# Kernel tuning notes

Hardware: AMD Instinct MI355X
Metric: run time of the kernel (lower is better)

## Reference

```python
import jax, jax.numpy as jnp
import numpy as np

B, N, T, FM = 2, 768, 96, 8
HID = 64
TD = HID // 2   # temporal_dim = max(8, 32) = 32
MD = HID // 2   # mark_hidden_dim = 32


def _lin_init(key, fan_in, fan_out):
    k1, k2 = jax.random.split(key)
    bound = 1.0 / np.sqrt(fan_in)
    w = jax.random.uniform(k1, (fan_in, fan_out), minval=-bound, maxval=bound, dtype=jnp.float32)
    b = jax.random.uniform(k2, (fan_out,), minval=-bound, maxval=bound, dtype=jnp.float32)
    return w, b


def setup_inputs() -> dict:
    key = jax.random.key(0)
    ks = jax.random.split(key, 16)
    x_hist = jax.random.normal(ks[0], (B, N, T), dtype=jnp.float32)
    x_mark = jax.random.normal(ks[1], (B, N, T, FM), dtype=jnp.float32)
    a_static = jax.random.uniform(ks[2], (N, N), dtype=jnp.float32)
    te_w1, te_b1 = _lin_init(ks[3], 3, TD)
    te_w2, te_b2 = _lin_init(ks[4], TD, TD)
    me_w1, me_b1 = _lin_init(ks[5], FM, MD)
    me_w2, me_b2 = _lin_init(ks[6], MD, MD)
    nf_w, nf_b = _lin_init(ks[7], TD + MD, HID)
    ps_w1, ps_b1 = _lin_init(ks[8], 3 * HID, HID)
    ps_w2, ps_b2 = _lin_init(ks[9], HID, 1)
    raw_lambda = jnp.array([np.log(0.1 / 0.9)], dtype=jnp.float32)  # logit(lambda_init)
    return dict(x_hist=x_hist, x_mark=x_mark, a_static=a_static,
                te_w1=te_w1, te_b1=te_b1, te_w2=te_w2, te_b2=te_b2,
                me_w1=me_w1, me_b1=me_b1, me_w2=me_w2, me_b2=me_b2,
                nf_w=nf_w, nf_b=nf_b,
                ps_w1=ps_w1, ps_b1=ps_b1, ps_w2=ps_w2, ps_b2=ps_b2,
                raw_lambda=raw_lambda)


def reference(x_hist, x_mark, a_static,
              te_w1, te_b1, te_w2, te_b2,
              me_w1, me_b1, me_w2, me_b2,
              nf_w, nf_b, ps_w1, ps_b1, ps_w2, ps_b2, raw_lambda):
    n = x_hist.shape[1]
    # temporal stats: last / mean / max over T -> [B,N,3]
    stats = jnp.stack([x_hist[:, :, -1], x_hist.mean(axis=-1), x_hist.max(axis=-1)], axis=-1)
    h_t = jax.nn.relu(stats @ te_w1 + te_b1) @ te_w2 + te_b2          # [B,N,TD]
    mark_sum = x_mark.mean(axis=2)                                    # [B,N,FM]
    h_m = jax.nn.relu(mark_sum @ me_w1 + me_b1) @ me_w2 + me_b2       # [B,N,MD]
    h = jax.nn.relu(jnp.concatenate([h_t, h_m], axis=-1) @ nf_w + nf_b)  # [B,N,H]
    # pair scorer: Linear([h_i, h_j, |h_i-h_j|]) decomposed over the 3 blocks
    hdim = h.shape[-1]
    w_i, w_j, w_d = ps_w1[:hdim], ps_w1[hdim:2 * hdim], ps_w1[2 * hdim:]
    s_i = h @ w_i                                                     # [B,N,H]
    s_j = h @ w_j                                                     # [B,N,H]
    diff = jnp.abs(h[:, :, None, :] - h[:, None, :, :])               # [B,N,N,H]
    pre = s_i[:, :, None, :] + s_j[:, None, :, :] + diff @ w_d + ps_b1
    delta = jnp.tanh((jax.nn.relu(pre) @ ps_w2 + ps_b2)[..., 0])      # [B,N,N]
    eye = jnp.eye(n, dtype=delta.dtype)
    delta = delta * (1.0 - eye)
    delta = 0.5 * (delta + jnp.swapaxes(delta, 1, 2))                 # sym_graph
    lam = jax.nn.sigmoid(raw_lambda)                                  # [1]
    a_hybrid = a_static[None] + lam * delta
    a_hybrid = jax.nn.relu(a_hybrid)                                  # nonneg_mode='relu'
    d = jnp.clip(a_hybrid.sum(axis=-1, keepdims=True), 1e-6, None)    # row norm
    a_hybrid = a_hybrid / d
    return a_hybrid, lam
```

## Files before the change

kernel.cpp:

```cpp
#include <hip/hip_runtime.h>
#include <hip/hip_bf16.h>
#include <math.h>

#define B_ 2
#define N_ 768
#define T_ 96
#define FM_ 8
#define HID_ 64
#define TD_ 32
#define MD_ 32
#define TILE 16
#define NTILES (N_/TILE)
#define NTP (NTILES*(NTILES+1)/2)
#define SSTR 68

typedef __attribute__((ext_vector_type(8))) short short8v;
typedef __attribute__((ext_vector_type(4))) float f32x4;
typedef __attribute__((ext_vector_type(4))) unsigned int uint4v;

__device__ __forceinline__ unsigned int pack_bf2(float d0, float d1){
  __hip_bfloat162 t = __float22bfloat162_rn(make_float2(d0, d1));
  unsigned int u;
  __builtin_memcpy(&u, &t, 4);
  return u;
}

__device__ __forceinline__ float ftanh(float x){
  float e = __expf(2.f * x);
  return 1.f - 2.f * __builtin_amdgcn_rcpf(e + 1.f);
}

__device__ __forceinline__ float wave_sum64(float v){
  #pragma unroll
  for (int m = 32; m; m >>= 1) v += __shfl_xor(v, m);
  return v;
}
__device__ __forceinline__ float wave_max64(float v){
  #pragma unroll
  for (int m = 32; m; m >>= 1) v = fmaxf(v, __shfl_xor(v, m));
  return v;
}

__global__ __launch_bounds__(64) void feat_kernel(
    const float* __restrict__ x_hist, const float* __restrict__ x_mark,
    const float* __restrict__ te_w1, const float* __restrict__ te_b1,
    const float* __restrict__ te_w2, const float* __restrict__ te_b2,
    const float* __restrict__ me_w1, const float* __restrict__ me_b1,
    const float* __restrict__ me_w2, const float* __restrict__ me_b2,
    const float* __restrict__ nf_w,  const float* __restrict__ nf_b,
    const float* __restrict__ ps_w1,
    float* __restrict__ h_out, float* __restrict__ si_out, float* __restrict__ sj_out,
    unsigned short* __restrict__ wdf)
{
  const int lane = threadIdx.x;

  if (blockIdx.x >= B_ * N_) {
    const int q  = blockIdx.x - B_ * N_;
    const int nt = q >> 1, s = q & 1;
    const int col = (lane & 15) + 16 * nt;
    const int k0  = s * 32 + ((lane >> 4) << 3);
    #pragma unroll
    for (int jj = 0; jj < 8; ++jj) {
      float v = ps_w1[(2 * HID_ + k0 + jj) * HID_ + col];
      __hip_bfloat16 bv = __float2bfloat16(v);
      unsigned short us;
      __builtin_memcpy(&us, &bv, 2);
      wdf[(q * 64 + lane) * 8 + jj] = us;
    }
    return;
  }

  const int row = blockIdx.x;

  __shared__ float st[3];
  __shared__ float ms[FM_];
  __shared__ float t1s[TD_];
  __shared__ float m1s[MD_];
  __shared__ float hc[HID_];
  __shared__ float hs[HID_];

  const float* xh = x_hist + (long)row * T_;
  float s  = xh[lane];
  float mx = s;
  if (lane < T_ - 64) { float v = xh[lane + 64]; s += v; mx = fmaxf(mx, v); }
  s  = wave_sum64(s);
  mx = wave_max64(mx);
  if (lane == 0) { st[0] = xh[T_ - 1]; st[1] = s * (1.0f / T_); st[2] = mx; }

  const float* xm = x_mark + (long)row * T_ * FM_;
  float msv = 0.f;
  #pragma unroll
  for (int k = 0; k < 12; ++k) msv += xm[lane + 64 * k];
  msv += __shfl_xor(msv, 8);
  msv += __shfl_xor(msv, 16);
  msv += __shfl_xor(msv, 32);
  if (lane < FM_) ms[lane] = msv * (1.0f / T_);
  __syncthreads();

  if (lane < TD_) {
    float a = te_b1[lane];
    #pragma unroll
    for (int k = 0; k < 3; ++k) a += st[k] * te_w1[k * TD_ + lane];
    t1s[lane] = fmaxf(a, 0.f);
    float am = me_b1[lane];
    #pragma unroll
    for (int k = 0; k < FM_; ++k) am += ms[k] * me_w1[k * MD_ + lane];
    m1s[lane] = fmaxf(am, 0.f);
  }
  __syncthreads();
  if (lane < TD_) {
    float a = te_b2[lane];
    #pragma unroll
    for (int k = 0; k < TD_; ++k) a += t1s[k] * te_w2[k * TD_ + lane];
    hc[lane] = a;
    float am = me_b2[lane];
    #pragma unroll
    for (int k = 0; k < MD_; ++k) am += m1s[k] * me_w2[k * MD_ + lane];
    hc[TD_ + lane] = am;
  }
  __syncthreads();
  {
    float a = nf_b[lane];
    #pragma unroll
    for (int k = 0; k < HID_; ++k) a += hc[k] * nf_w[k * HID_ + lane];
    float hv = fmaxf(a, 0.f);
    hs[lane] = hv;
    h_out[(long)row * HID_ + lane] = hv;
  }
  __syncthreads();
  {
    float a1 = 0.f, a2 = 0.f;
    #pragma unroll
    for (int k = 0; k < HID_; ++k) {
      float hv = hs[k];
      a1 += hv * ps_w1[k * HID_ + lane];
      a2 += hv * ps_w1[(HID_ + k) * HID_ + lane];
    }
    si_out[(long)row * HID_ + lane] = a1;
    sj_out[(long)row * HID_ + lane] = a2;
  }
}

__global__ __launch_bounds__(256) void pair_kernel(
    const float* __restrict__ h, const float* __restrict__ si, const float* __restrict__ sj,
    const float* __restrict__ ps_b1, const float* __restrict__ ps_w2,
    const float* __restrict__ ps_b2, const unsigned short* __restrict__ wdf,
    float* __restrict__ delta)
{
  int bidx = blockIdx.x;
  int b  = bidx / NTP;
  int tp = bidx % NTP;
  int tI = 0;
  while (tp >= NTILES - tI) { tp -= NTILES - tI; ++tI; }
  int tJ = tI + tp;
  const int i0 = tI * TILE, j0 = tJ * TILE;

  __shared__ float hI  [TILE][HID_];
  __shared__ float hJT [HID_][TILE + 1];
  __shared__ float SIIb[TILE][SSTR];
  __shared__ float SJI_[TILE][SSTR];
  __shared__ float SIJb[TILE][SSTR];
  __shared__ float SJJ_[TILE][SSTR];
  __shared__ float w2s [HID_];

  const int tid  = threadIdx.x;
  const int lane = tid & 63;
  const int w    = tid >> 6;

  {
    const int r  = tid >> 4;
    const int c4 = (tid & 15) * 4;
    const f32x4 b14 = *(const f32x4*)(ps_b1 + c4);
    const long gi = ((long)b * N_ + i0 + r) * HID_ + c4;
    const long gj = ((long)b * N_ + j0 + r) * HID_ + c4;
    f32x4 vhi = *(const f32x4*)(h  + gi);
    f32x4 vhj = *(const f32x4*)(h  + gj);
    f32x4 vii = *(const f32x4*)(si + gi);
    f32x4 vji = *(const f32x4*)(sj + gi);
    f32x4 vij = *(const f32x4*)(si + gj);
    f32x4 vjj = *(const f32x4*)(sj + gj);
    *(f32x4*)&hI  [r][c4] = vhi;
    #pragma unroll
    for (int q = 0; q < 4; ++q) hJT[c4 + q][r] = vhj[q];
    *(f32x4*)&SIIb[r][c4] = vii + b14;
    *(f32x4*)&SJI_[r][c4] = vji;
    *(f32x4*)&SIJb[r][c4] = vij + b14;
    *(f32x4*)&SJJ_[r][c4] = vjj;
    if (tid < 16) *(f32x4*)&w2s[tid * 4] = *(const f32x4*)(ps_w2 + tid * 4);
  }
  const float b2 = ps_b2[0];
  __syncthreads();

  const int g   = lane >> 4;
  const int c16 = lane & 15;

  short8v wfr[8];
  const short8v* wdp = (const short8v*)wdf;
  #pragma unroll
  for (int q = 0; q < 8; ++q) wfr[q] = wdp[q * 64 + lane];

  float hJv[2][8];
  #pragma unroll
  for (int s = 0; s < 2; ++s)
    #pragma unroll
    for (int jj = 0; jj < 8; ++jj)
      hJv[s][jj] = hJT[32 * s + 8 * g + jj][c16];

  float* drow = delta + (long)b * N_ * N_;

  #pragma unroll
  for (int m = 0; m < 4; ++m) {
    const int iloc = w * 4 + m;
    const int i = i0 + iloc;

    short8v afr[2];
    #pragma unroll
    for (int s = 0; s < 2; ++s) {
      f32x4 ha = *(const f32x4*)&hI[iloc][32 * s + 8 * g];
      f32x4 hb = *(const f32x4*)&hI[iloc][32 * s + 8 * g + 4];
      uint4v uv;
      #pragma unroll
      for (int p = 0; p < 2; ++p) {
        float d0 = fabsf(ha[2*p]   - hJv[s][2*p]);
        float d1 = fabsf(ha[2*p+1] - hJv[s][2*p+1]);
        uv[p] = pack_bf2(d0, d1);
      }
      #pragma unroll
      for (int p = 0; p < 2; ++p) {
        float d0 = fabsf(hb[2*p]   - hJv[s][4 + 2*p]);
        float d1 = fabsf(hb[2*p+1] - hJv[s][4 + 2*p+1]);
        uv[2 + p] = pack_bf2(d0, d1);
      }
      afr[s] = __builtin_bit_cast(short8v, uv);
    }

    f32x4 acc[4];
    #pragma unroll
    for (int mt = 0; mt < 4; ++mt) acc[mt] = (f32x4){0.f, 0.f, 0.f, 0.f};
    #pragma unroll
    for (int s = 0; s < 2; ++s)
      #pragma unroll
      for (int mt = 0; mt < 4; ++mt)
        acc[mt] = __builtin_amdgcn_mfma_f32_16x16x32_bf16(wfr[2 * mt + s], afr[s], acc[mt], 0, 0, 0);

    float a1 = 0.f, a2 = 0.f;
    #pragma unroll
    for (int mt = 0; mt < 4; ++mt) {
      const int cb = 16 * mt + 4 * g;
      f32x4 sII4 = *(const f32x4*)&SIIb[iloc][cb];
      f32x4 sJI4 = *(const f32x4*)&SJI_[iloc][cb];
      f32x4 sJJ4 = *(const f32x4*)&SJJ_[c16][cb];
      f32x4 sIJ4 = *(const f32x4*)&SIJb[c16][cb];
      f32x4 w24  = *(const f32x4*)&w2s[cb];
      #pragma unroll
      for (int r = 0; r < 4; ++r) {
        float av = acc[mt][r];
        a1 += fmaxf(av + sII4[r] + sJJ4[r], 0.f) * w24[r];
        a2 += fmaxf(av + sJI4[r] + sIJ4[r], 0.f) * w24[r];
      }
    }
    a1 += __shfl_xor(a1, 16);  a1 += __shfl_xor(a1, 32);
    a2 += __shfl_xor(a2, 16);  a2 += __shfl_xor(a2, 32);

    if (g == 0) {
      const int j = j0 + c16;
      float sym = 0.5f * (ftanh(a1 + b2) + ftanh(a2 + b2));
      float val = (i == j) ? 0.f : sym;
      drow[(long)i * N_ + j] = val;
      drow[(long)j * N_ + i] = val;
    }
  }
}

__global__ __launch_bounds__(256) void norm_kernel(
    const float* __restrict__ a_static, const float* __restrict__ raw_lambda,
    float* __restrict__ out)
{
  const int row = blockIdx.x;
  const int i   = row % N_;
  const int tid = threadIdx.x;
  const float lam = 1.f / (1.f + expf(-raw_lambda[0]));

  const float* arow = a_static + (long)i * N_;
  float* drow = out + (long)row * N_;

  float vals[3];
  float s = 0.f;
  #pragma unroll
  for (int r = 0; r < 3; ++r) {
    int j = r * 256 + tid;
    float v = arow[j] + lam * drow[j];
    v = fmaxf(v, 0.f);
    vals[r] = v;
    s += v;
  }
  s = wave_sum64(s);
  __shared__ float ps[4];
  if ((tid & 63) == 0) ps[tid >> 6] = s;
  __syncthreads();
  float tot = ps[0] + ps[1] + ps[2] + ps[3];
  float inv = 1.f / fmaxf(tot, 1e-6f);
  #pragma unroll
  for (int r = 0; r < 3; ++r) {
    int j = r * 256 + tid;
    drow[j] = vals[r] * inv;
  }
  if (row == 0 && tid == 0) out[(long)B_ * N_ * N_] = lam;
}

extern "C" void kernel_launch(void* const* d_in, const int* in_sizes, int n_in,
                              void* d_out, int out_size, void* d_ws, size_t ws_size,
                              hipStream_t stream) {
  const float* x_hist     = (const float*)d_in[0];
  const float* x_mark     = (const float*)d_in[1];
  const float* a_static   = (const float*)d_in[2];
  const float* te_w1      = (const float*)d_in[3];
  const float* te_b1      = (const float*)d_in[4];
  const float* te_w2      = (const float*)d_in[5];
  const float* te_b2      = (const float*)d_in[6];
  const float* me_w1      = (const float*)d_in[7];
  const float* me_b1      = (const float*)d_in[8];
  const float* me_w2      = (const float*)d_in[9];
  const float* me_b2      = (const float*)d_in[10];
  const float* nf_w       = (const float*)d_in[11];
  const float* nf_b       = (const float*)d_in[12];
  const float* ps_w1      = (const float*)d_in[13];
  const float* ps_b1      = (const float*)d_in[14];
  const float* ps_w2      = (const float*)d_in[15];
  const float* ps_b2      = (const float*)d_in[16];
  const float* raw_lambda = (const float*)d_in[17];

  float* out = (float*)d_out;
  float* h   = (float*)d_ws;
  float* si  = h  + (long)B_ * N_ * HID_;
  float* sj  = si + (long)B_ * N_ * HID_;
  unsigned short* wdf = (unsigned short*)(sj + (long)B_ * N_ * HID_);

  feat_kernel<<<B_ * N_ + 8, 64, 0, stream>>>(
      x_hist, x_mark, te_w1, te_b1, te_w2, te_b2,
      me_w1, me_b1, me_w2, me_b2, nf_w, nf_b, ps_w1, h, si, sj, wdf);

  pair_kernel<<<B_ * NTP, 256, 0, stream>>>(
      h, si, sj, ps_b1, ps_w2, ps_b2, wdf, out);

  norm_kernel<<<B_ * N_, 256, 0, stream>>>(a_static, raw_lambda, out);
}
```

Before: 35.97 us.

## Use 32x16 pair tiles with hoisted per-column operands in pair kernel

The pair kernel now covers a 32-row by 16-column tile per block, so each wave handles 8 rows instead of 4. The grid is re-enumerated over upper-triangular 32x16 tiles, giving 600 blocks per batch instead of 1176. The column-side scorer terms and w2 fragments are loaded into registers once, outside the row loop, and a launch-bounds occupancy hint is added. Writes are restricted to i<j plus the diagonal, which removes duplicate stores from tiles that straddle the diagonal. The costs are more registers, more shared memory per block, and fewer blocks available to spread across the GPU.

Measured after the change: 35.60 us. Within noise of the previous version (-1.0%).

```diff
diff --git a/kernel.cpp b/kernel.cpp
--- a/kernel.cpp
+++ b/kernel.cpp
@@ -10,8 +10,9 @@
 #define TD_ 32
 #define MD_ 32
 #define TILE 16
+#define TI32 32
 #define NTILES (N_/TILE)
-#define NTP (NTILES*(NTILES+1)/2)
+#define PERB 600
 #define SSTR 68
 
 typedef __attribute__((ext_vector_type(8))) short short8v;
@@ -141,24 +142,24 @@
   }
 }
 
-__global__ __launch_bounds__(256) void pair_kernel(
+__global__ __launch_bounds__(256, 3) void pair_kernel(
     const float* __restrict__ h, const float* __restrict__ si, const float* __restrict__ sj,
     const float* __restrict__ ps_b1, const float* __restrict__ ps_w2,
     const float* __restrict__ ps_b2, const unsigned short* __restrict__ wdf,
     float* __restrict__ delta)
 {
   int bidx = blockIdx.x;
-  int b  = bidx / NTP;
-  int tp = bidx % NTP;
-  int tI = 0;
-  while (tp >= NTILES - tI) { tp -= NTILES - tI; ++tI; }
-  int tJ = tI + tp;
-  const int i0 = tI * TILE, j0 = tJ * TILE;
-
-  __shared__ float hI  [TILE][HID_];
+  int b = bidx / PERB;
+  int t = bidx % PERB;
+  int a = 0;
+  while (t >= NTILES - 2 * a) { t -= NTILES - 2 * a; ++a; }
+  int tJ = 2 * a + t;
+  const int i0 = a * TI32, j0 = tJ * TILE;
+
+  __shared__ float hI  [TI32][HID_];
   __shared__ float hJT [HID_][TILE + 1];
-  __shared__ float SIIb[TILE][SSTR];
-  __shared__ float SJI_[TILE][SSTR];
+  __shared__ float SIIb[TI32][SSTR];
+  __shared__ float SJI_[TI32][SSTR];
   __shared__ float SIJb[TILE][SSTR];
   __shared__ float SJJ_[TILE][SSTR];
   __shared__ float w2s [HID_];
@@ -171,21 +172,20 @@
     const int r  = tid >> 4;
     const int c4 = (tid & 15) * 4;
     const f32x4 b14 = *(const f32x4*)(ps_b1 + c4);
-    const long gi = ((long)b * N_ + i0 + r) * HID_ + c4;
+    #pragma unroll
+    for (int p = 0; p < 2; ++p) {
+      const int rr = r + p * 16;
+      const long gi = ((long)b * N_ + i0 + rr) * HID_ + c4;
+      *(f32x4*)&hI  [rr][c4] = *(const f32x4*)(h  + gi);
+      *(f32x4*)&SIIb[rr][c4] = *(const f32x4*)(si + gi) + b14;
+      *(f32x4*)&SJI_[rr][c4] = *(const f32x4*)(sj + gi);
+    }
     const long gj = ((long)b * N_ + j0 + r) * HID_ + c4;
-    f32x4 vhi = *(const f32x4*)(h  + gi);
-    f32x4 vhj = *(const f32x4*)(h  + gj);
-    f32x4 vii = *(const f32x4*)(si + gi);
-    f32x4 vji = *(const f32x4*)(sj + gi);
-    f32x4 vij = *(const f32x4*)(si + gj);
-    f32x4 vjj = *(const f32x4*)(sj + gj);
-    *(f32x4*)&hI  [r][c4] = vhi;
+    f32x4 vhj = *(const f32x4*)(h + gj);
     #pragma unroll
     for (int q = 0; q < 4; ++q) hJT[c4 + q][r] = vhj[q];
-    *(f32x4*)&SIIb[r][c4] = vii + b14;
-    *(f32x4*)&SJI_[r][c4] = vji;
-    *(f32x4*)&SIJb[r][c4] = vij + b14;
-    *(f32x4*)&SJJ_[r][c4] = vjj;
+    *(f32x4*)&SIJb[r][c4] = *(const f32x4*)(si + gj) + b14;
+    *(f32x4*)&SJJ_[r][c4] = *(const f32x4*)(sj + gj);
     if (tid < 16) *(f32x4*)&w2s[tid * 4] = *(const f32x4*)(ps_w2 + tid * 4);
   }
   const float b2 = ps_b2[0];
@@ -206,11 +206,20 @@
     for (int jj = 0; jj < 8; ++jj)
       hJv[s][jj] = hJT[32 * s + 8 * g + jj][c16];
 
+  f32x4 sJJ4h[4], sIJ4h[4], w24h[4];
+  #pragma unroll
+  for (int mt = 0; mt < 4; ++mt) {
+    const int cb = 16 * mt + 4 * g;
+    sJJ4h[mt] = *(const f32x4*)&SJJ_[c16][cb];
+    sIJ4h[mt] = *(const f32x4*)&SIJb[c16][cb];
+    w24h[mt]  = *(const f32x4*)&w2s[cb];
+  }
+
   float* drow = delta + (long)b * N_ * N_;
 
   #pragma unroll
-  for (int m = 0; m < 4; ++m) {
-    const int iloc = w * 4 + m;
+  for (int m = 0; m < 8; ++m) {
+    const int iloc = w * 8 + m;
     const int i = i0 + iloc;
 
     short8v afr[2];
@@ -249,14 +258,11 @@
       const int cb = 16 * mt + 4 * g;
       f32x4 sII4 = *(const f32x4*)&SIIb[iloc][cb];
       f32x4 sJI4 = *(const f32x4*)&SJI_[iloc][cb];
-      f32x4 sJJ4 = *(const f32x4*)&SJJ_[c16][cb];
-      f32x4 sIJ4 = *(const f32x4*)&SIJb[c16][cb];
-      f32x4 w24  = *(const f32x4*)&w2s[cb];
       #pragma unroll
       for (int r = 0; r < 4; ++r) {
         float av = acc[mt][r];
-        a1 += fmaxf(av + sII4[r] + sJJ4[r], 0.f) * w24[r];
-        a2 += fmaxf(av + sJI4[r] + sIJ4[r], 0.f) * w24[r];
+        a1 += fmaxf(av + sII4[r] + sJJ4h[mt][r], 0.f) * w24h[mt][r];
+        a2 += fmaxf(av + sJI4[r] + sIJ4h[mt][r], 0.f) * w24h[mt][r];
       }
     }
     a1 += __shfl_xor(a1, 16);  a1 += __shfl_xor(a1, 32);
@@ -264,10 +270,13 @@
 
     if (g == 0) {
       const int j = j0 + c16;
-      float sym = 0.5f * (ftanh(a1 + b2) + ftanh(a2 + b2));
-      float val = (i == j) ? 0.f : sym;
-      drow[(long)i * N_ + j] = val;
-      drow[(long)j * N_ + i] = val;
+      if (i < j) {
+        float sym = 0.5f * (ftanh(a1 + b2) + ftanh(a2 + b2));
+        drow[(long)i * N_ + j] = sym;
+        drow[(long)j * N_ + i] = sym;
+      } else if (i == j) {
+        drow[(long)i * N_ + i] = 0.f;
+      }
     }
   }
 }
@@ -340,7 +349,7 @@
       x_hist, x_mark, te_w1, te_b1, te_w2, te_b2,
       me_w1, me_b1, me_w2, me_b2, nf_w, nf_b, ps_w1, h, si, sj, wdf);
 
-  pair_kernel<<<B_ * NTP, 256, 0, stream>>>(
+  pair_kernel<<<B_ * PERB, 256, 0, stream>>>(
       h, si, sj, ps_b1, ps_w2, ps_b2, wdf, out);
 
   norm_kernel<<<B_ * N_, 256, 0, stream>>>(a_static, raw_lambda, out);
```
